# Optimization experiments

Measured on AMD Instinct MI355X. Metric: run time of the kernel, lower is better.

## Reference

```python
import jax, jax.numpy as jnp
import numpy as np
import math

B, S, D, H = 2, 2048, 2048, 16
HD = D // H  # head_dim = 128
NEG = -9e15


def setup_inputs() -> dict:
    key = jax.random.key(0)
    k1, k2, k3 = jax.random.split(key, 3)
    x = jax.random.normal(k1, (B, S, D), dtype=jnp.float32)
    Wqkv = jax.random.normal(k2, (D, 3 * D), dtype=jnp.float32) * (1.0 / math.sqrt(D))
    bqkv = jnp.zeros((3 * D,), dtype=jnp.float32)
    Wo = jax.random.normal(k3, (D, D), dtype=jnp.float32) * (1.0 / math.sqrt(D))
    bo = jnp.zeros((D,), dtype=jnp.float32)
    return {"x": x, "Wqkv": Wqkv, "bqkv": bqkv, "Wo": Wo, "bo": bo}


def reference(x, Wqkv, bqkv, Wo, bo):
    b, s, d = x.shape
    # fused QKV projection
    qkv = x @ Wqkv + bqkv                       # [B,S,3D]
    qkv = qkv.reshape(b, s, H, 3 * HD)          # per-head interleaved q|k|v
    qkv = qkv.transpose(0, 2, 1, 3)             # [B,H,S,3*HD]
    q, k, v = jnp.split(qkv, 3, axis=-1)        # each [B,H,S,HD]
    scale = 1.0 / math.sqrt(HD)
    logits = jnp.einsum('bhqd,bhkd->bhqk', q, k) * scale  # [B,H,S,S]
    causal = jnp.tril(jnp.ones((s, s), dtype=bool))[None, None]
    logits = jnp.where(causal, logits, NEG)
    score = jax.nn.softmax(logits, axis=-1)
    attn = jnp.einsum('bhqk,bhkd->bhqd', score, v)         # [B,H,S,HD]
    attn = attn.transpose(0, 2, 1, 3).reshape(b, s, d)
    return attn @ Wo + bo
```

## Files before the change

### kernel.cpp

```cpp
#include <hip/hip_runtime.h>
#include <stdint.h>

#define DEV static __device__ __forceinline__

typedef _Float16 half8 __attribute__((ext_vector_type(8)));
typedef _Float16 half4 __attribute__((ext_vector_type(4)));
typedef float f32x4 __attribute__((ext_vector_type(4)));
typedef uint16_t u16x8 __attribute__((ext_vector_type(8)));

constexpr int Bc = 2, Sc = 2048, Dc = 2048, Hc = 16, HDc = 128;
constexpr int D3c = 3 * Dc;
constexpr int Mc = Bc * Sc;

DEV void gl_lds16(const void* g, void* l) {
    __builtin_amdgcn_global_load_lds(
        (const __attribute__((address_space(1))) unsigned int*)g,
        (__attribute__((address_space(3))) unsigned int*)l,
        16, 0, 0);
}

__global__ __launch_bounds__(256) void cast_f16_kernel(
    const float* __restrict__ in, _Float16* __restrict__ out)
{
    int i = blockIdx.x * 256 + threadIdx.x;
    const float4* p = (const float4*)in;
    float4 a = p[i * 2], b = p[i * 2 + 1];
    half8 hv;
    hv[0] = (_Float16)a.x; hv[1] = (_Float16)a.y; hv[2] = (_Float16)a.z; hv[3] = (_Float16)a.w;
    hv[4] = (_Float16)b.x; hv[5] = (_Float16)b.y; hv[6] = (_Float16)b.z; hv[7] = (_Float16)b.w;
    *(half8*)(out + (size_t)i * 8) = hv;
}

__global__ __launch_bounds__(256) void transpose_cast_kernel(
    const float* __restrict__ in, _Float16* __restrict__ out, int R, int C)
{
    __shared__ float ls[64][64];
    const int t = threadIdx.x;
    const int r0 = blockIdx.y * 64, c0 = blockIdx.x * 64;
    {
        const int rr = t >> 4, lc = t & 15;
#pragma unroll
        for (int p = 0; p < 4; ++p) {
            int r = p * 16 + rr;
            int pc = lc ^ ((r >> 3) & 7);
            *(float4*)&ls[r][pc * 4] =
                *(const float4*)&in[(size_t)(r0 + r) * C + c0 + lc * 4];
        }
    }
    __syncthreads();
    {
        const int oc = t >> 3, ss = (t & 7) * 8;
#pragma unroll
        for (int p = 0; p < 2; ++p) {
            int c = p * 32 + oc;
            int lc = c >> 2, wi = c & 3;
            half8 hv;
#pragma unroll
            for (int j = 0; j < 8; ++j) {
                int r = ss + j;
                hv[j] = (_Float16)ls[r][(lc ^ ((r >> 3) & 7)) * 4 + wi];
            }
            *(half8*)&out[(size_t)(c0 + c) * R + r0 + ss] = hv;
        }
    }
}

__global__ __launch_bounds__(256) void transpose_v_kernel(
    const uint16_t* __restrict__ qkv, uint16_t* __restrict__ vt)
{
    __shared__ uint16_t ls[64][64];
    const int t = threadIdx.x;
    const int s0 = blockIdx.x * 64, d0 = blockIdx.y * 64, bh = blockIdx.z;
    const int b = bh >> 4, h = bh & 15;
    {
        const int sr = t >> 3, lc = t & 7;
#pragma unroll
        for (int p = 0; p < 2; ++p) {
            int s = p * 32 + sr;
            int pc = lc ^ ((s >> 3) & 7);
            *(u16x8*)&ls[s][pc * 8] =
                *(const u16x8*)&qkv[(size_t)(b * Sc + s0 + s) * D3c + h * 384 + 256 + d0 + lc * 8];
        }
    }
    __syncthreads();
    {
        const int od = t >> 3, ss = (t & 7) * 8;
#pragma unroll
        for (int p = 0; p < 2; ++p) {
            int d = p * 32 + od;
            int lc = d >> 3, wi = d & 7;
            u16x8 hv;
#pragma unroll
            for (int j = 0; j < 8; ++j) {
                int s = ss + j;
                hv[j] = ls[s][(lc ^ ((s >> 3) & 7)) * 8 + wi];
            }
            *(u16x8*)&vt[(size_t)(bh * HDc + d0 + d) * Sc + s0 + ss] = hv;
        }
    }
}

template <int BF16OUT>
__global__ __launch_bounds__(256, 2) void gemm_bt_kernel(
    const _Float16* __restrict__ A, const _Float16* __restrict__ Bt,
    const float* __restrict__ bias, void* __restrict__ Cout,
    int M, int N, int K)
{
    __shared__ __align__(16) char smem[65536];
    const int t = threadIdx.x, w = t >> 6, lane = t & 63;
    const int quad = lane >> 4, l15 = lane & 15;
    const int wr = w >> 1, wc = w & 1;
    const int n0 = blockIdx.x * 128, m0 = blockIdx.y * 128;

    char *cA = smem,         *cB = smem + 16384;
    char *nA = smem + 32768, *nB = smem + 49152;

    const f32x4 vzero = {0.f, 0.f, 0.f, 0.f};
    f32x4 acc[4][4];
#pragma unroll
    for (int i = 0; i < 4; ++i)
#pragma unroll
        for (int j = 0; j < 4; ++j) acc[i][j] = vzero;

    auto stage = [&](char* dA, char* dB, int kk) {
#pragma unroll
        for (int i = 0; i < 4; ++i) {
            int c = i * 256 + t;
            int row = c >> 3, kbs = c & 7, kact = kbs ^ (row & 7);
            gl_lds16(A + (size_t)(m0 + row) * K + kk * 64 + kact * 8,
                     dA + (i * 256 + w * 64) * 16);
        }
#pragma unroll
        for (int i = 0; i < 4; ++i) {
            int c = i * 256 + t;
            int row = c >> 3, kbs = c & 7, kact = kbs ^ (row & 7);
            gl_lds16(Bt + (size_t)(n0 + row) * K + kk * 64 + kact * 8,
                     dB + (i * 256 + w * 64) * 16);
        }
    };

    const int kiters = K >> 6;
    stage(cA, cB, 0);
    __syncthreads();

    for (int kt = 0; kt < kiters; ++kt) {
        const bool more = (kt + 1 < kiters);
        if (more) stage(nA, nB, kt + 1);

#pragma unroll
        for (int ks = 0; ks < 2; ++ks) {
            half8 af[4], bf[4];
#pragma unroll
            for (int mt = 0; mt < 4; ++mt) {
                int row = wr * 64 + mt * 16 + l15;
                int kact = (ks * 4 + quad) ^ (l15 & 7);
                af[mt] = *(const half8*)(cA + row * 128 + kact * 16);
            }
#pragma unroll
            for (int nt = 0; nt < 4; ++nt) {
                int row = wc * 64 + nt * 16 + l15;
                int kact = (ks * 4 + quad) ^ (l15 & 7);
                bf[nt] = *(const half8*)(cB + row * 128 + kact * 16);
            }
#pragma unroll
            for (int mt = 0; mt < 4; ++mt)
#pragma unroll
                for (int nt = 0; nt < 4; ++nt)
                    acc[mt][nt] = __builtin_amdgcn_mfma_f32_16x16x32_f16(
                        af[mt], bf[nt], acc[mt][nt], 0, 0, 0);
        }

        if (more) {
            __syncthreads();
            char* tp;
            tp = cA; cA = nA; nA = tp;
            tp = cB; cB = nB; nB = tp;
        }
    }

#pragma unroll
    for (int nt = 0; nt < 4; ++nt) {
        int col = n0 + wc * 64 + nt * 16 + l15;
        float bv = bias[col];
#pragma unroll
        for (int mt = 0; mt < 4; ++mt)
#pragma unroll
            for (int r = 0; r < 4; ++r) {
                int row = m0 + wr * 64 + mt * 16 + quad * 4 + r;
                float v = acc[mt][nt][r] + bv;
                if (BF16OUT) ((_Float16*)Cout)[(size_t)row * N + col] = (_Float16)v;
                else         ((float*)Cout)[(size_t)row * N + col] = v;
            }
    }
}

__global__ __launch_bounds__(256, 4) void flash_kernel(
    const _Float16* __restrict__ qkv, const _Float16* __restrict__ vt,
    _Float16* __restrict__ attn)
{
    __shared__ __align__(16) char smem[32768];
    char* sK = smem;
    char* sV = smem + 16384;

    const int t = threadIdx.x, w = t >> 6, lane = t & 63;
    const int quad = lane >> 4, l15 = lane & 15;
    const int bh = blockIdx.x;
    const int qt = 31 - blockIdx.y;
    const int b = bh >> 4, h = bh & 15;
    const int q0 = qt * 64;
    const int qrow = q0 + w * 16 + l15;

    half8 qf[4];
#pragma unroll
    for (int ks = 0; ks < 4; ++ks) {
        const _Float16* p = qkv + (size_t)(b * Sc + qrow) * D3c +
                            h * 384 + ks * 32 + quad * 8;
        qf[ks] = *(const half8*)p;
    }

    const f32x4 vzero = {0.f, 0.f, 0.f, 0.f};
    f32x4 o[8];
#pragma unroll
    for (int dt = 0; dt < 8; ++dt) o[dt] = vzero;
    float m_st = -1e30f, l_st = 0.f;

    const float kScale = 0.08838834764831845f * 1.4426950408889634f;
    const int nkt = qt + 1;

    for (int kt = 0; kt < nkt; ++kt) {
#pragma unroll
        for (int i = 0; i < 4; ++i) {
            int c = i * 256 + t;
            int row = c >> 4, kbs = c & 15, kact = kbs ^ (row & 15);
            gl_lds16(qkv + (size_t)(b * Sc + kt * 64 + row) * D3c + h * 384 + 128 + kact * 8,
                     sK + (i * 256 + w * 64) * 16);
        }
#pragma unroll
        for (int i = 0; i < 4; ++i) {
            int c = i * 256 + t;
            int row = c >> 3, kbs = c & 7, kact = kbs ^ (row & 7);
            gl_lds16(vt + (size_t)(bh * HDc + row) * Sc + kt * 64 + kact * 8,
                     sV + (i * 256 + w * 64) * 16);
        }
        __syncthreads();

        f32x4 sf[4];
#pragma unroll
        for (int kb = 0; kb < 4; ++kb) sf[kb] = vzero;
#pragma unroll
        for (int ks = 0; ks < 4; ++ks) {
#pragma unroll
            for (int kb = 0; kb < 4; ++kb) {
                int row = kb * 16 + l15;
                int slot = (ks * 4 + quad) ^ l15;
                half8 kf = *(const half8*)(sK + row * 256 + slot * 16);
                sf[kb] = __builtin_amdgcn_mfma_f32_16x16x32_f16(kf, qf[ks], sf[kb], 0, 0, 0);
            }
        }

        const bool domask = (kt == qt);
        float rm = -1e30f;
#pragma unroll
        for (int kb = 0; kb < 4; ++kb)
#pragma unroll
            for (int r = 0; r < 4; ++r) {
                float v = sf[kb][r] * kScale;
                if (domask) {
                    int col = kt * 64 + kb * 16 + quad * 4 + r;
                    if (col > qrow) v = -1e30f;
                }
                sf[kb][r] = v;
                rm = fmaxf(rm, v);
            }
        rm = fmaxf(rm, __shfl_xor(rm, 16, 64));
        rm = fmaxf(rm, __shfl_xor(rm, 32, 64));
        float mn = fmaxf(m_st, rm);
        float alpha = __builtin_amdgcn_exp2f(m_st - mn);
        m_st = mn;

        half4 pb[4];
        float rs = 0.f;
#pragma unroll
        for (int kb = 0; kb < 4; ++kb)
#pragma unroll
            for (int r = 0; r < 4; ++r) {
                float p = __builtin_amdgcn_exp2f(sf[kb][r] - mn);
                rs += p;
                pb[kb][r] = (_Float16)p;
            }
        rs += __shfl_xor(rs, 16, 64);
        rs += __shfl_xor(rs, 32, 64);
        l_st = l_st * alpha + rs;

#pragma unroll
        for (int dt = 0; dt < 8; ++dt)
#pragma unroll
            for (int r = 0; r < 4; ++r) o[dt][r] *= alpha;

#pragma unroll
        for (int kb = 0; kb < 4; ++kb) {
#pragma unroll
            for (int dt = 0; dt < 8; ++dt) {
                int row = dt * 16 + l15;
                int slot = (kb * 2 + (quad >> 1)) ^ (l15 & 7);
                half4 vf = *(const half4*)(sV + row * 128 + slot * 16 + (quad & 1) * 8);
                o[dt] = __builtin_amdgcn_mfma_f32_16x16x16f16(vf, pb[kb], o[dt], 0, 0, 0);
            }
        }
        __syncthreads();
    }

    char* sO = smem;
    float linv = 1.0f / l_st;
#pragma unroll
    for (int dt = 0; dt < 8; ++dt) {
        half4 hv;
#pragma unroll
        for (int r = 0; r < 4; ++r) hv[r] = (_Float16)(o[dt][r] * linv);
        *(half4*)(sO + (w * 16 + l15) * 272 + (dt * 16 + quad * 4) * 2) = hv;
    }
    __syncthreads();
#pragma unroll
    for (int i = 0; i < 4; ++i) {
        int q = i * 16 + (t >> 4);
        int d = (t & 15) * 8;
        half8 hv = *(const half8*)(sO + q * 272 + d * 2);
        *(half8*)(attn + (size_t)(b * Sc + q0 + q) * Dc + h * HDc + d) = hv;
    }
}

extern "C" void kernel_launch(void* const* d_in, const int* in_sizes, int n_in,
                              void* d_out, int out_size, void* d_ws, size_t ws_size,
                              hipStream_t stream)
{
    (void)in_sizes; (void)n_in; (void)out_size; (void)ws_size;
    const float* x    = (const float*)d_in[0];
    const float* Wqkv = (const float*)d_in[1];
    const float* bqkv = (const float*)d_in[2];
    const float* Wo   = (const float*)d_in[3];
    const float* bo   = (const float*)d_in[4];
    float* out = (float*)d_out;

    _Float16* xb  = (_Float16*)d_ws;
    _Float16* wt1 = xb  + (size_t)Mc * Dc;
    _Float16* wt2 = wt1 + (size_t)D3c * Dc;
    _Float16* qkv = wt2 + (size_t)Dc * Dc;
    _Float16* vtg  = wt1;
    _Float16* attn = xb;

    cast_f16_kernel<<<Mc * Dc / 2048, 256, 0, stream>>>(x, xb);
    transpose_cast_kernel<<<dim3(D3c / 64, Dc / 64), 256, 0, stream>>>(Wqkv, wt1, Dc, D3c);
    transpose_cast_kernel<<<dim3(Dc / 64, Dc / 64), 256, 0, stream>>>(Wo, wt2, Dc, Dc);
    gemm_bt_kernel<1><<<dim3(D3c / 128, Mc / 128), 256, 0, stream>>>(
        xb, wt1, bqkv, qkv, Mc, D3c, Dc);
    transpose_v_kernel<<<dim3(Sc / 64, 2, Bc * Hc), 256, 0, stream>>>(
        (const uint16_t*)qkv, (uint16_t*)vtg);
    flash_kernel<<<dim3(Bc * Hc, 32), 256, 0, stream>>>(qkv, vtg, attn);
    gemm_bt_kernel<0><<<dim3(Dc / 128, Mc / 128), 256, 0, stream>>>(
        attn, wt2, bo, out, Mc, Dc, Dc);
}
```

Baseline: 379.3 us.

## Single-buffer GEMM LDS, swizzle workgroup order, raise priority around attention MFMAs

The GEMM kernel drops double-buffered LDS (64KB to 32KB) and loads each K-tile synchronously with two barriers per iteration, so more workgroups can fit per CU. It also remaps block IDs with a stride-8 swizzle, presumably to spread neighbouring tiles across XCDs or improve L2 reuse. The attention kernel wraps its MFMA sections in s_setprio to favour matrix issue across co-resident waves. The cost is that the GEMM no longer overlaps global-to-LDS loads with compute inside a block, and depends on occupancy to hide that latency.

```diff
diff --git a/kernel.cpp b/kernel.cpp
--- a/kernel.cpp
+++ b/kernel.cpp
@@ -106,14 +106,18 @@
     const float* __restrict__ bias, void* __restrict__ Cout,
     int M, int N, int K)
 {
-    __shared__ __align__(16) char smem[65536];
+    __shared__ __align__(16) char smem[32768];
+    char* sA = smem;
+    char* sB = smem + 16384;
     const int t = threadIdx.x, w = t >> 6, lane = t & 63;
     const int quad = lane >> 4, l15 = lane & 15;
     const int wr = w >> 1, wc = w & 1;
-    const int n0 = blockIdx.x * 128, m0 = blockIdx.y * 128;
-
-    char *cA = smem,         *cB = smem + 16384;
-    char *nA = smem + 32768, *nB = smem + 49152;
+
+    const int nwg = gridDim.x * gridDim.y;
+    const int wg  = blockIdx.y * gridDim.x + blockIdx.x;
+    const int swz = (wg & 7) * (nwg >> 3) + (wg >> 3);
+    const int bx  = swz % gridDim.x, by = swz / gridDim.x;
+    const int n0 = bx * 128, m0 = by * 128;
 
     const f32x4 vzero = {0.f, 0.f, 0.f, 0.f};
     f32x4 acc[4][4];
@@ -122,31 +126,23 @@
 #pragma unroll
         for (int j = 0; j < 4; ++j) acc[i][j] = vzero;
 
-    auto stage = [&](char* dA, char* dB, int kk) {
+    const int kiters = K >> 6;
+    for (int kk = 0; kk < kiters; ++kk) {
 #pragma unroll
         for (int i = 0; i < 4; ++i) {
             int c = i * 256 + t;
             int row = c >> 3, kbs = c & 7, kact = kbs ^ (row & 7);
             gl_lds16(A + (size_t)(m0 + row) * K + kk * 64 + kact * 8,
-                     dA + (i * 256 + w * 64) * 16);
+                     sA + (i * 256 + w * 64) * 16);
         }
 #pragma unroll
         for (int i = 0; i < 4; ++i) {
             int c = i * 256 + t;
             int row = c >> 3, kbs = c & 7, kact = kbs ^ (row & 7);
             gl_lds16(Bt + (size_t)(n0 + row) * K + kk * 64 + kact * 8,
-                     dB + (i * 256 + w * 64) * 16);
-        }
-    };
-
-    const int kiters = K >> 6;
-    stage(cA, cB, 0);
-    __syncthreads();
-
-    for (int kt = 0; kt < kiters; ++kt) {
-        const bool more = (kt + 1 < kiters);
-        if (more) stage(nA, nB, kt + 1);
-
+                     sB + (i * 256 + w * 64) * 16);
+        }
+        __syncthreads();
 #pragma unroll
         for (int ks = 0; ks < 2; ++ks) {
             half8 af[4], bf[4];
@@ -154,13 +150,13 @@
             for (int mt = 0; mt < 4; ++mt) {
                 int row = wr * 64 + mt * 16 + l15;
                 int kact = (ks * 4 + quad) ^ (l15 & 7);
-                af[mt] = *(const half8*)(cA + row * 128 + kact * 16);
+                af[mt] = *(const half8*)(sA + row * 128 + kact * 16);
             }
 #pragma unroll
             for (int nt = 0; nt < 4; ++nt) {
                 int row = wc * 64 + nt * 16 + l15;
                 int kact = (ks * 4 + quad) ^ (l15 & 7);
-                bf[nt] = *(const half8*)(cB + row * 128 + kact * 16);
+                bf[nt] = *(const half8*)(sB + row * 128 + kact * 16);
             }
 #pragma unroll
             for (int mt = 0; mt < 4; ++mt)
@@ -169,13 +165,7 @@
                     acc[mt][nt] = __builtin_amdgcn_mfma_f32_16x16x32_f16(
                         af[mt], bf[nt], acc[mt][nt], 0, 0, 0);
         }
-
-        if (more) {
-            __syncthreads();
-            char* tp;
-            tp = cA; cA = nA; nA = tp;
-            tp = cB; cB = nB; nB = tp;
-        }
+        __syncthreads();
     }
 
 #pragma unroll
@@ -247,6 +237,7 @@
         f32x4 sf[4];
 #pragma unroll
         for (int kb = 0; kb < 4; ++kb) sf[kb] = vzero;
+        __builtin_amdgcn_s_setprio(1);
 #pragma unroll
         for (int ks = 0; ks < 4; ++ks) {
 #pragma unroll
@@ -257,6 +248,7 @@
                 sf[kb] = __builtin_amdgcn_mfma_f32_16x16x32_f16(kf, qf[ks], sf[kb], 0, 0, 0);
             }
         }
+        __builtin_amdgcn_s_setprio(0);
 
         const bool domask = (kt == qt);
         float rm = -1e30f;
@@ -297,6 +289,7 @@
 #pragma unroll
             for (int r = 0; r < 4; ++r) o[dt][r] *= alpha;
 
+        __builtin_amdgcn_s_setprio(1);
 #pragma unroll
         for (int kb = 0; kb < 4; ++kb) {
 #pragma unroll
@@ -307,6 +300,7 @@
                 o[dt] = __builtin_amdgcn_mfma_f32_16x16x16f16(vf, pb[kb], o[dt], 0, 0, 0);
             }
         }
+        __builtin_amdgcn_s_setprio(0);
         __syncthreads();
     }
 
```

Result: no change. 381.4 us (+0.5%).
